# Kernel optimization log

Hardware: AMD Instinct MI355X
Metric: run time of the kernel (lower is better)

The kernel has to match this reference:

```python
import jax, jax.numpy as jnp
import numpy as np

B, M, N = 64, 100, 100
LAMBDA_COORD = 1.0
LAMBDA_CONF = 1.0
EPS = 1e-12


def _hungarian(cost):
    """O(n^3) Hungarian algorithm (potentials / e-maxx variant) on a square
    numpy cost matrix. Returns row_to_col assignment (length n)."""
    n = cost.shape[0]
    u = np.zeros(n + 1)
    v = np.zeros(n + 1)
    p = np.zeros(n + 1, dtype=np.int64)   # p[j] = row matched to column j
    way = np.zeros(n + 1, dtype=np.int64)
    for i in range(1, n + 1):
        p[0] = i
        j0 = 0
        minv = np.full(n + 1, np.inf)
        used = np.zeros(n + 1, dtype=bool)
        while True:
            used[j0] = True
            i0 = p[j0]
            js = np.nonzero(~used)[0]
            js = js[js > 0]
            cur = cost[i0 - 1, js - 1] - u[i0] - v[js]
            upd = cur < minv[js]
            minv[js] = np.where(upd, cur, minv[js])
            way[js] = np.where(upd, j0, way[js])
            j1 = js[np.argmin(minv[js])]
            delta = minv[j1]
            uj = np.nonzero(used)[0]
            u[p[uj]] += delta
            v[uj] -= delta
            minv[js] -= delta
            j0 = j1
            if p[j0] == 0:
                break
        while j0:
            j1 = way[j0]
            p[j0] = p[j1]
            j0 = j1
    row_to_col = np.full(n, -1, dtype=np.int64)
    for j in range(1, n + 1):
        row_to_col[p[j] - 1] = j - 1
    return row_to_col


def _match(pred_xy, target_xy, target_conf):
    """Host-side matching (mirrors the original's CPU round trip).
    Returns padded rows [B,P], cols [B,P] (cols index into the ORIGINAL target
    axis) and cnt [B] = number of matched pairs (min(M, K_valid))."""
    Bb, Mm, _ = pred_xy.shape
    Nn = target_xy.shape[1]
    P = min(Mm, Nn)
    rows = np.zeros((Bb, P), np.int64)
    cols = np.zeros((Bb, P), np.int64)
    cnt = np.zeros(Bb, np.int64)
    for b in range(Bb):
        valid = np.nonzero(target_conf[b] > 0.5)[0]
        K = valid.size
        if K == 0:
            continue
        tgt = target_xy[b, valid]                       # [K,2]
        cost = np.linalg.norm(pred_xy[b][:, None, :] - tgt[None, :, :], axis=-1)  # [M,K]
        n = max(Mm, K)
        sq = np.zeros((n, n))                           # zero-pad to square
        sq[:Mm, :K] = cost
        r2c = _hungarian(sq)
        k = 0
        for r in range(Mm):
            c = r2c[r]
            if 0 <= c < K:
                rows[b, k] = r
                cols[b, k] = valid[c]
                k += 1
        cnt[b] = k
    return rows, cols, cnt


def _loss(pred, target, rows, cols, cnt):
    Bb, P = rows.shape
    bidx = jnp.arange(Bb)[:, None]
    mp = pred[bidx, rows]                                # [B,P,3] matched preds
    mt = target[bidx, cols]                              # [B,P,3] matched tgts
    mask = (jnp.arange(P)[None, :] < cnt[:, None]).astype(pred.dtype)
    denom = jnp.maximum(cnt, 1).astype(pred.dtype)
    # per-batch F.mse_loss: mean over cnt*2 coord elements
    se = (((mp[..., :2] - mt[..., :2]) ** 2).sum(-1) * mask).sum(-1)
    loss_coord = jnp.where(cnt > 0, se / (2.0 * denom), 0.0).sum()
    # per-batch F.binary_cross_entropy: mean over cnt elements
    pconf = jnp.clip(mp[..., 2], EPS, 1.0 - EPS)
    tconf = mt[..., 2]
    bce = -(tconf * jnp.log(pconf) + (1.0 - tconf) * jnp.log1p(-pconf))
    loss_conf = jnp.where(cnt > 0, (bce * mask).sum(-1) / denom, 0.0).sum()
    return (LAMBDA_COORD * loss_coord + LAMBDA_CONF * loss_conf) / Bb


def setup_inputs() -> dict:
    key = jax.random.key(0)
    k1, k2 = jax.random.split(key)
    pred = jax.random.uniform(k1, (B, M, 3), dtype=jnp.float32)
    target = jax.random.uniform(k2, (B, N, 3), dtype=jnp.float32)
    return {"pred": pred, "target": target}


def reference(pred, target):
    pred_np = np.asarray(pred)
    tgt_np = np.asarray(target)
    rows, cols, cnt = _match(pred_np[..., :2], tgt_np[..., :2], tgt_np[..., 2])
    rows = jnp.asarray(rows)
    cols = jnp.asarray(cols)
    cnt = jnp.asarray(cnt)
    return _loss(pred, target, rows, cols, cnt)
```

## Files before the change

kernel.cpp:

```cpp
#include <hip/hip_runtime.h>
#include <math.h>

#define BATCH 64
#define MM 100
#define NN 100
#define ST 101
#define BIGCLAIM 0x7fffffff


__device__ __forceinline__ int readlane_i(int v, int lane) {
    return __builtin_amdgcn_readlane(v, lane);
}
__device__ __forceinline__ float readlane_f(float v, int lane) {
    return __int_as_float(__builtin_amdgcn_readlane(__float_as_int(v), lane));
}

template<int CTRL>
__device__ __forceinline__ float dpp_min_f32(float x) {
    int p = __builtin_amdgcn_update_dpp(__float_as_int(x), __float_as_int(x),
                                        CTRL, 0xF, 0xF, false);
    return fminf(x, __int_as_float(p));
}
__device__ __forceinline__ float wave_min_f32(float x) {
    x = dpp_min_f32<0xB1>(x);
    x = dpp_min_f32<0x4E>(x);
    x = dpp_min_f32<0x141>(x);
    x = dpp_min_f32<0x140>(x);
    x = dpp_min_f32<0x142>(x);
    x = dpp_min_f32<0x143>(x);
    return readlane_f(x, 63);
}


__global__ __launch_bounds__(128) void hungarian_loss_kernel(
        const float* __restrict__ pred, const float* __restrict__ target,
        double* __restrict__ ws) {
    const int b    = blockIdx.x;
    const int tid  = threadIdx.x;
    const int lane = tid & 63;
    const int wave = tid >> 6;
    const float* P = pred + b * MM * 3;
    const float* T = target + b * NN * 3;

    __shared__ float px[MM], py[MM], pc[MM];
    __shared__ float tvx[NN], tvy[NN], tvc[NN];
    __shared__ float Tc[NN * ST];
    __shared__ int   rmini[NN];
    __shared__ int   claimArr[MM + 1];
    __shared__ int   Ksh;

    float pxA = P[3*lane], pyA = P[3*lane+1];
    float pxB = 0.f, pyB = 0.f;
    const bool colBvalid = (lane + 64 < MM);
    if (colBvalid) { pxB = P[3*(lane+64)]; pyB = P[3*(lane+64)+1]; }

    if (wave == 0) {
        px[lane] = pxA; py[lane] = pyA; pc[lane] = P[3*lane+2];
        if (colBvalid) { px[lane+64]=pxB; py[lane+64]=pyB; pc[lane+64]=P[3*(lane+64)+2]; }
        float cxA=0.f, cyA=0.f, ccA=0.f, cxB=0.f, cyB=0.f, ccB=0.f;
        bool vA_=false, vB_=false;
        { cxA=T[3*lane]; cyA=T[3*lane+1]; ccA=T[3*lane+2]; vA_ = ccA > 0.5f; }
        if (lane + 64 < NN) {
            cxB=T[3*(lane+64)]; cyB=T[3*(lane+64)+1]; ccB=T[3*(lane+64)+2];
            vB_ = ccB > 0.5f;
        }
        unsigned long long mAv = __ballot(vA_);
        unsigned long long mBv = __ballot(vB_);
        int nA_ = __popcll(mAv);
        int K0  = nA_ + __popcll(mBv);
        unsigned long long below = (1ull << lane) - 1ull;
        if (vA_) { int q = __popcll(mAv & below);       tvx[q]=cxA; tvy[q]=cyA; tvc[q]=ccA; }
        if (vB_) { int q = nA_ + __popcll(mBv & below); tvx[q]=cxB; tvy[q]=cyB; tvc[q]=ccB; }
        if (lane == 0) Ksh = K0;
        claimArr[lane] = BIGCLAIM;
        if (lane + 64 <= MM) claimArr[lane + 64] = BIGCLAIM;
    }
    __syncthreads();
    const int K = Ksh;
    if (K == 0) { if (tid == 0) ws[b] = 0.0; return; }

    float txA = (lane < K)      ? tvx[lane]      : 0.f;
    float tyA = (lane < K)      ? tvy[lane]      : 0.f;
    float txB = (lane + 64 < K) ? tvx[lane + 64] : 0.f;
    float tyB = (lane + 64 < K) ? tvy[lane + 64] : 0.f;

    for (int c = wave; c < K; c += 2) {
        float tx = (c < 64) ? readlane_f(txA, c) : readlane_f(txB, c - 64);
        float ty = (c < 64) ? readlane_f(tyA, c) : readlane_f(tyB, c - 64);
        float dxA = __fsub_rn(pxA, tx), dyA = __fsub_rn(pyA, ty);
        float cA = __fsqrt_rn(__fadd_rn(__fmul_rn(dxA,dxA), __fmul_rn(dyA,dyA)));
        Tc[c*ST + lane] = cA;
        float cB = 1e30f;
        if (colBvalid) {
            float dxB = __fsub_rn(pxB, tx), dyB = __fsub_rn(pyB, ty);
            cB = __fsqrt_rn(__fadd_rn(__fmul_rn(dxB,dxB), __fmul_rn(dyB,dyB)));
            Tc[c*ST + lane + 64] = cB;
        }
        float m = wave_min_f32(fminf(cA, cB));
        unsigned long long eA = __ballot(cA == m);
        unsigned long long eB = __ballot(cB == m);
        int argc = eA ? ((int)__ffsll(eA) - 1) : ((int)__ffsll(eB) - 1 + 64);
        if (lane == 0) rmini[c] = argc;
    }
    __syncthreads();
    if (wave == 1) return;

    const float INF32 = __builtin_inff();
    const int jA = lane;
    const int jB = lane + 64;
    const bool validB = (jB <= MM);
    const int idxA = (jA >= 1) ? (jA - 1) : 0;
    const int idxB = validB ? (jB - 1) : (MM - 1);

    int rA = lane + 1, rB = lane + 65;
    int argA = 0, argB = 0;
    if (lane < K)      { argA = rmini[lane] + 1;      atomicMin(&claimArr[argA], rA); }
    if (lane + 64 < K) { argB = rmini[lane + 64] + 1; atomicMin(&claimArr[argB], rB); }
    __threadfence_block();
    int pA = 0, pB = 0;
    if (jA >= 1) { int c0 = claimArr[jA]; pA = (c0 != BIGCLAIM) ? c0 : 0; }
    if (validB)  { int c0 = claimArr[jB]; pB = (c0 != BIGCLAIM) ? c0 : 0; }
    bool freeA = (lane < K)      && (claimArr[argA] != rA);
    bool freeB = (lane + 64 < K) && (claimArr[argB] != rB);
    unsigned long long fA = __ballot(freeA);
    unsigned long long fB = __ballot(freeB);

    float vvA = 0.f, vvB = 0.f;

    unsigned long long dijA = 0ull, dijB = 0ull;
    for (int sweep = 0; sweep < 2; ++sweep) {
        unsigned long long curA = fA, curB = fB;
        fA = 0ull; fB = 0ull;
        while (curA | curB) {
            int r;
            if (curA) { r = (int)__ffsll(curA);      curA &= curA - 1; }
            else      { r = (int)__ffsll(curB) + 64; curB &= curB - 1; }

            float cA = Tc[(r-1)*ST + idxA];
            float cB = Tc[(r-1)*ST + idxB];
            float rcA = (jA >= 1) ? (cA - vvA) : INF32;
            float rcB = validB ? (cB - vvB) : INF32;
            float m1 = wave_min_f32(fminf(rcA, rcB));
            unsigned long long eA = __ballot(rcA == m1);
            unsigned long long eB = __ballot(rcB == m1);
            int j1 = eA ? ((int)__ffsll(eA) - 1) : ((int)__ffsll(eB) - 1 + 64);

            float rcA2 = (jA == j1) ? INF32 : rcA;
            float rcB2 = (jB == j1) ? INF32 : rcB;
            float m2 = wave_min_f32(fminf(rcA2, rcB2));

            int holder = (j1 < 64) ? readlane_i(pA, j1) : readlane_i(pB, j1 & 63);

            if (m1 < m2) {
                float dv = m2 - m1;
                if (jA == j1) { vvA -= dv; pA = r; }
                if (validB && jB == j1) { vvB -= dv; pB = r; }
                if (holder != 0) {
                    if (sweep == 0) {
                        if (holder <= 64) fA |= 1ull << (holder - 1);
                        else              fB |= 1ull << (holder - 65);
                    } else {
                        if (holder <= 64) dijA |= 1ull << (holder - 1);
                        else              dijB |= 1ull << (holder - 65);
                    }
                }
            } else {
                if (holder == 0) {
                    if (jA == j1) pA = r;
                    if (validB && jB == j1) pB = r;
                } else {
                    unsigned long long e2A = __ballot(rcA2 == m2);
                    unsigned long long e2B = __ballot(rcB2 == m2);
                    int j2 = e2A ? ((int)__ffsll(e2A) - 1)
                                 : ((int)__ffsll(e2B) - 1 + 64);
                    int h2 = (j2 < 64) ? readlane_i(pA, j2)
                                       : readlane_i(pB, j2 & 63);
                    if (h2 == 0) {
                        if (jA == j2) pA = r;
                        if (validB && jB == j2) pB = r;
                    } else {
                        if (sweep == 0) {
                            if (r <= 64) fA |= 1ull << (r - 1);
                            else         fB |= 1ull << (r - 65);
                        } else {
                            if (r <= 64) dijA |= 1ull << (r - 1);
                            else         dijB |= 1ull << (r - 65);
                        }
                    }
                }
            }
        }
    }

    while (dijA | dijB) {
        int r;
        if (dijA) { r = (int)__ffsll(dijA);      dijA &= dijA - 1; }
        else      { r = (int)__ffsll(dijB) + 64; dijB &= dijB - 1; }

        float minvA = INF32, minvB = INF32;
        int wayA = 0, wayB = 0;
        bool usedA = (lane == 0), usedB = false;
        float dpopA = 0.f, dpopB = 0.f;
        if (lane == 0) pA = r;
        int j0 = 0, jfree = -1;
        float dstar = 0.f;

        float cA_f = Tc[(r-1)*ST + idxA];
        float cB_f = Tc[(r-1)*ST + idxB];
        float S = 0.f;

        for (int it = 0; it <= MM; ++it) {
            float candA = INF32, candB = INF32;
            if (jA >= 1 && !usedA) {
                float t = (cA_f - vvA) + S;
                if (t < minvA) { minvA = t; wayA = j0; }
                candA = minvA;
            }
            if (validB && !usedB) {
                float t = (cB_f - vvB) + S;
                if (t < minvB) { minvB = t; wayB = j0; }
                candB = minvB;
            }

            float delta = wave_min_f32(fminf(candA, candB));
            unsigned long long eA = __ballot(candA == delta);
            unsigned long long eB = __ballot(candB == delta);
            int j1 = eA ? ((int)__ffsll(eA) - 1) : ((int)__ffsll(eB) - 1 + 64);

            if (jA == j1) { usedA = true; dpopA = delta; }
            if (jB == j1) { usedB = true; dpopB = delta; }

            int pa = readlane_i(pA, j1 & 63);
            int pb = readlane_i(pB, j1 & 63);
            int pj1 = (j1 < 64) ? pa : pb;
            if (pj1 == 0) { jfree = j1; dstar = delta; break; }

            float nxA = Tc[(pj1-1)*ST + idxA];
            float nxB = Tc[(pj1-1)*ST + idxB];
            float cjm = (j1 < 64) ? readlane_f(nxA, j1) : readlane_f(nxB, j1 & 63);
            float vjm = (j1 < 64) ? readlane_f(vvA, j1) : readlane_f(vvB, j1 & 63);
            S = (delta - cjm) + vjm;
            cA_f = nxA; cB_f = nxB;
            j0 = j1;
        }

        if (usedA && jA >= 1) vvA += dpopA - dstar;
        if (usedB)            vvB += dpopB - dstar;

        int jc = jfree;
        for (int s = 0; s <= MM && jc > 0; ++s) {
            int wa = readlane_i(wayA, jc & 63);
            int wb = readlane_i(wayB, jc & 63);
            int w  = (jc < 64) ? wa : wb;
            int pa = readlane_i(pA, w & 63);
            int pb = readlane_i(pB, w & 63);
            int pw = (w < 64) ? pa : pb;
            if (jA == jc) pA = pw;
            if (jB == jc) pB = pw;
            jc = w;
        }
    }

    double se = 0.0, bce = 0.0;
    if (jA >= 1 && pA > 0) {
        int rr = jA - 1, c = pA - 1;
        float dx = __fsub_rn(px[rr], tvx[c]);
        float dy = __fsub_rn(py[rr], tvy[c]);
        se = (double)dx*(double)dx + (double)dy*(double)dy;
        double pcv = (double)pc[rr];
        pcv = fmin(fmax(pcv, 1e-12), 1.0 - 1e-12);
        double tc = (double)tvc[c];
        bce = -(tc * log(pcv) + (1.0 - tc) * log1p(-pcv));
    }
    if (validB && pB > 0) {
        int rr = jB - 1, c = pB - 1;
        float dx = __fsub_rn(px[rr], tvx[c]);
        float dy = __fsub_rn(py[rr], tvy[c]);
        se += (double)dx*(double)dx + (double)dy*(double)dy;
        double pcv = (double)pc[rr];
        pcv = fmin(fmax(pcv, 1e-12), 1.0 - 1e-12);
        double tc = (double)tvc[c];
        bce += -(tc * log(pcv) + (1.0 - tc) * log1p(-pcv));
    }
    for (int m = 1; m < 64; m <<= 1) {
        se  += __shfl_xor(se,  m, 64);
        bce += __shfl_xor(bce, m, 64);
    }
    if (lane == 0) ws[b] = se / (2.0 * (double)K) + bce / (double)K;
}

__global__ __launch_bounds__(64) void final_reduce(const double* __restrict__ ws,
                                                   float* __restrict__ out) {
    double v = ws[threadIdx.x];
    for (int m = 1; m < 64; m <<= 1) v += __shfl_xor(v, m, 64);
    if (threadIdx.x == 0) out[0] = (float)(v / (double)BATCH);
}

extern "C" void kernel_launch(void* const* d_in, const int* in_sizes, int n_in,
                              void* d_out, int out_size, void* d_ws, size_t ws_size,
                              hipStream_t stream) {
    const float* pred   = (const float*)d_in[0];
    const float* target = (const float*)d_in[1];
    double* ws = (double*)d_ws;
    float* out = (float*)d_out;
    hungarian_loss_kernel<<<dim3(BATCH), dim3(128), 0, stream>>>(pred, target, ws);
    final_reduce<<<dim3(1), dim3(64), 0, stream>>>(ws, out);
}
```

Measured before the change: 53.63 us.

## Split Hungarian kernel into two stages and use packed-key wave argmin

Replaces the float wave-min plus ballot argmin with a single unsigned min over packed keys (order-preserving float bits with the low 7 bits replaced by the column index). The auction sweep now always takes the second-best value instead of branching on ties. The kernel is split into a stage that builds costs and runs the auction and a stage that rebuilds the cost matrix and runs Dijkstra augmentation, passing state through workspace memory. This cuts the number of reductions per step but adds a launch, recomputes the cost matrix, and truncates key precision, which can change tie-breaking and the final matching.

```diff
diff --git a/kernel.cpp b/kernel.cpp
--- a/kernel.cpp
+++ b/kernel.cpp
@@ -6,6 +6,8 @@
 #define NN 100
 #define ST 101
 #define BIGCLAIM 0x7fffffff
+#define WS_STATE_OFF 512
+#define WS_STRIDE   1024
 
 
 __device__ __forceinline__ int readlane_i(int v, int lane) {
@@ -15,26 +17,31 @@
     return __int_as_float(__builtin_amdgcn_readlane(__float_as_int(v), lane));
 }
 
+__device__ __forceinline__ unsigned pack_key(float x, int col) {
+    unsigned u = __float_as_uint(x);
+    u ^= ((unsigned)((int)u >> 31)) | 0x80000000u;
+    return (u & 0xFFFFFF80u) | (unsigned)col;
+}
+
 template<int CTRL>
-__device__ __forceinline__ float dpp_min_f32(float x) {
-    int p = __builtin_amdgcn_update_dpp(__float_as_int(x), __float_as_int(x),
-                                        CTRL, 0xF, 0xF, false);
-    return fminf(x, __int_as_float(p));
-}
-__device__ __forceinline__ float wave_min_f32(float x) {
-    x = dpp_min_f32<0xB1>(x);
-    x = dpp_min_f32<0x4E>(x);
-    x = dpp_min_f32<0x141>(x);
-    x = dpp_min_f32<0x140>(x);
-    x = dpp_min_f32<0x142>(x);
-    x = dpp_min_f32<0x143>(x);
-    return readlane_f(x, 63);
-}
-
-
-__global__ __launch_bounds__(128) void hungarian_loss_kernel(
+__device__ __forceinline__ unsigned dpp_min_u32(unsigned x) {
+    int p = __builtin_amdgcn_update_dpp((int)x, (int)x, CTRL, 0xF, 0xF, false);
+    unsigned up = (unsigned)p;
+    return (x < up) ? x : up;
+}
+__device__ __forceinline__ unsigned wave_min_u32(unsigned x) {
+    x = dpp_min_u32<0xB1>(x);
+    x = dpp_min_u32<0x4E>(x);
+    x = dpp_min_u32<0x141>(x);
+    x = dpp_min_u32<0x140>(x);
+    x = dpp_min_u32<0x142>(x);
+    x = dpp_min_u32<0x143>(x);
+    return (unsigned)readlane_i((int)x, 63);
+}
+
+__global__ __launch_bounds__(128) void hung_stage1(
         const float* __restrict__ pred, const float* __restrict__ target,
-        double* __restrict__ ws) {
+        char* __restrict__ wsbase) {
     const int b    = blockIdx.x;
     const int tid  = threadIdx.x;
     const int lane = tid & 63;
@@ -42,8 +49,7 @@
     const float* P = pred + b * MM * 3;
     const float* T = target + b * NN * 3;
 
-    __shared__ float px[MM], py[MM], pc[MM];
-    __shared__ float tvx[NN], tvy[NN], tvc[NN];
+    __shared__ float tvx[NN], tvy[NN];
     __shared__ float Tc[NN * ST];
     __shared__ int   rmini[NN];
     __shared__ int   claimArr[MM + 1];
@@ -54,30 +60,30 @@
     const bool colBvalid = (lane + 64 < MM);
     if (colBvalid) { pxB = P[3*(lane+64)]; pyB = P[3*(lane+64)+1]; }
 
+    int* st = (int*)(wsbase + WS_STATE_OFF + (size_t)b * WS_STRIDE);
+
     if (wave == 0) {
-        px[lane] = pxA; py[lane] = pyA; pc[lane] = P[3*lane+2];
-        if (colBvalid) { px[lane+64]=pxB; py[lane+64]=pyB; pc[lane+64]=P[3*(lane+64)+2]; }
-        float cxA=0.f, cyA=0.f, ccA=0.f, cxB=0.f, cyB=0.f, ccB=0.f;
-        bool vA_=false, vB_=false;
-        { cxA=T[3*lane]; cyA=T[3*lane+1]; ccA=T[3*lane+2]; vA_ = ccA > 0.5f; }
+        float cxA=T[3*lane], cyA=T[3*lane+1], ccA=T[3*lane+2];
+        bool vA_ = ccA > 0.5f;
+        float cxB=0.f, cyB=0.f; bool vB_=false;
         if (lane + 64 < NN) {
-            cxB=T[3*(lane+64)]; cyB=T[3*(lane+64)+1]; ccB=T[3*(lane+64)+2];
-            vB_ = ccB > 0.5f;
+            cxB=T[3*(lane+64)]; cyB=T[3*(lane+64)+1];
+            vB_ = T[3*(lane+64)+2] > 0.5f;
         }
         unsigned long long mAv = __ballot(vA_);
         unsigned long long mBv = __ballot(vB_);
         int nA_ = __popcll(mAv);
         int K0  = nA_ + __popcll(mBv);
         unsigned long long below = (1ull << lane) - 1ull;
-        if (vA_) { int q = __popcll(mAv & below);       tvx[q]=cxA; tvy[q]=cyA; tvc[q]=ccA; }
-        if (vB_) { int q = nA_ + __popcll(mBv & below); tvx[q]=cxB; tvy[q]=cyB; tvc[q]=ccB; }
+        if (vA_) { int q = __popcll(mAv & below);       tvx[q]=cxA; tvy[q]=cyA; }
+        if (vB_) { int q = nA_ + __popcll(mBv & below); tvx[q]=cxB; tvy[q]=cyB; }
         if (lane == 0) Ksh = K0;
         claimArr[lane] = BIGCLAIM;
         if (lane + 64 <= MM) claimArr[lane + 64] = BIGCLAIM;
     }
     __syncthreads();
     const int K = Ksh;
-    if (K == 0) { if (tid == 0) ws[b] = 0.0; return; }
+    if (K == 0) { if (tid == 0) st[0] = 0; return; }
 
     float txA = (lane < K)      ? tvx[lane]      : 0.f;
     float tyA = (lane < K)      ? tvy[lane]      : 0.f;
@@ -90,17 +96,16 @@
         float dxA = __fsub_rn(pxA, tx), dyA = __fsub_rn(pyA, ty);
         float cA = __fsqrt_rn(__fadd_rn(__fmul_rn(dxA,dxA), __fmul_rn(dyA,dyA)));
         Tc[c*ST + lane] = cA;
-        float cB = 1e30f;
+        unsigned kB = 0xFFFFFFFFu;
         if (colBvalid) {
             float dxB = __fsub_rn(pxB, tx), dyB = __fsub_rn(pyB, ty);
-            cB = __fsqrt_rn(__fadd_rn(__fmul_rn(dxB,dxB), __fmul_rn(dyB,dyB)));
+            float cB = __fsqrt_rn(__fadd_rn(__fmul_rn(dxB,dxB), __fmul_rn(dyB,dyB)));
             Tc[c*ST + lane + 64] = cB;
-        }
-        float m = wave_min_f32(fminf(cA, cB));
-        unsigned long long eA = __ballot(cA == m);
-        unsigned long long eB = __ballot(cB == m);
-        int argc = eA ? ((int)__ffsll(eA) - 1) : ((int)__ffsll(eB) - 1 + 64);
-        if (lane == 0) rmini[c] = argc;
+            kB = pack_key(cB, lane + 64);
+        }
+        unsigned kA = pack_key(cA, lane);
+        unsigned k = wave_min_u32(kA < kB ? kA : kB);
+        if (lane == 0) rmini[c] = (int)(k & 127u);
     }
     __syncthreads();
     if (wave == 1) return;
@@ -140,57 +145,125 @@
             float cB = Tc[(r-1)*ST + idxB];
             float rcA = (jA >= 1) ? (cA - vvA) : INF32;
             float rcB = validB ? (cB - vvB) : INF32;
-            float m1 = wave_min_f32(fminf(rcA, rcB));
-            unsigned long long eA = __ballot(rcA == m1);
-            unsigned long long eB = __ballot(rcB == m1);
-            int j1 = eA ? ((int)__ffsll(eA) - 1) : ((int)__ffsll(eB) - 1 + 64);
-
-            float rcA2 = (jA == j1) ? INF32 : rcA;
-            float rcB2 = (jB == j1) ? INF32 : rcB;
-            float m2 = wave_min_f32(fminf(rcA2, rcB2));
+            unsigned kA = pack_key(rcA, jA);
+            unsigned kB = pack_key(rcB, jB);
+            unsigned k1 = wave_min_u32(kA < kB ? kA : kB);
+            int j1 = (int)(k1 & 127u);
+            unsigned kA2 = (jA == j1) ? 0xFFFFFFFFu : kA;
+            unsigned kB2 = (jB == j1) ? 0xFFFFFFFFu : kB;
+            unsigned k2 = wave_min_u32(kA2 < kB2 ? kA2 : kB2);
+            int j2 = (int)(k2 & 127u);
+
+            float v1a = readlane_f(rcA, j1 & 63), v1b = readlane_f(rcB, j1 & 63);
+            float val1 = (j1 < 64) ? v1a : v1b;
+            float v2a = readlane_f(rcA, j2 & 63), v2b = readlane_f(rcB, j2 & 63);
+            float val2 = (j2 < 64) ? v2a : v2b;
+            float dv = fmaxf(val2 - val1, 0.f);
 
             int holder = (j1 < 64) ? readlane_i(pA, j1) : readlane_i(pB, j1 & 63);
-
-            if (m1 < m2) {
-                float dv = m2 - m1;
-                if (jA == j1) { vvA -= dv; pA = r; }
-                if (validB && jB == j1) { vvB -= dv; pB = r; }
-                if (holder != 0) {
-                    if (sweep == 0) {
-                        if (holder <= 64) fA |= 1ull << (holder - 1);
-                        else              fB |= 1ull << (holder - 65);
-                    } else {
-                        if (holder <= 64) dijA |= 1ull << (holder - 1);
-                        else              dijB |= 1ull << (holder - 65);
-                    }
-                }
-            } else {
-                if (holder == 0) {
-                    if (jA == j1) pA = r;
-                    if (validB && jB == j1) pB = r;
+            if (jA == j1) { vvA -= dv; pA = r; }
+            if (validB && jB == j1) { vvB -= dv; pB = r; }
+            if (holder != 0) {
+                if (sweep == 0) {
+                    if (holder <= 64) fA |= 1ull << (holder - 1);
+                    else              fB |= 1ull << (holder - 65);
                 } else {
-                    unsigned long long e2A = __ballot(rcA2 == m2);
-                    unsigned long long e2B = __ballot(rcB2 == m2);
-                    int j2 = e2A ? ((int)__ffsll(e2A) - 1)
-                                 : ((int)__ffsll(e2B) - 1 + 64);
-                    int h2 = (j2 < 64) ? readlane_i(pA, j2)
-                                       : readlane_i(pB, j2 & 63);
-                    if (h2 == 0) {
-                        if (jA == j2) pA = r;
-                        if (validB && jB == j2) pB = r;
-                    } else {
-                        if (sweep == 0) {
-                            if (r <= 64) fA |= 1ull << (r - 1);
-                            else         fB |= 1ull << (r - 65);
-                        } else {
-                            if (r <= 64) dijA |= 1ull << (r - 1);
-                            else         dijB |= 1ull << (r - 65);
-                        }
-                    }
+                    if (holder <= 64) dijA |= 1ull << (holder - 1);
+                    else              dijB |= 1ull << (holder - 65);
                 }
             }
         }
     }
+
+    if (lane == 0) {
+        st[0] = K;
+        *(unsigned long long*)(st + 2) = dijA;
+        *(unsigned long long*)(st + 4) = dijB;
+    }
+    int*   pArr  = st + 6;
+    float* vvArr = (float*)(st + 6 + 101);
+    pArr[lane] = pA;  vvArr[lane] = vvA;
+    if (validB) { pArr[jB] = pB; vvArr[jB] = vvB; }
+}
+
+__global__ __launch_bounds__(128) void hung_stage2(
+        const float* __restrict__ pred, const float* __restrict__ target,
+        char* __restrict__ wsbase, double* __restrict__ wsloss) {
+    const int b    = blockIdx.x;
+    const int tid  = threadIdx.x;
+    const int lane = tid & 63;
+    const int wave = tid >> 6;
+    const float* P = pred + b * MM * 3;
+    const float* T = target + b * NN * 3;
+
+    __shared__ float px[MM], py[MM], pc[MM];
+    __shared__ float tvx[NN], tvy[NN], tvc[NN];
+    __shared__ float Tc[NN * ST];
+    __shared__ int   Ksh;
+
+    float pxA = P[3*lane], pyA = P[3*lane+1];
+    float pxB = 0.f, pyB = 0.f;
+    const bool colBvalid = (lane + 64 < MM);
+    if (colBvalid) { pxB = P[3*(lane+64)]; pyB = P[3*(lane+64)+1]; }
+
+    const int* st = (const int*)(wsbase + WS_STATE_OFF + (size_t)b * WS_STRIDE);
+
+    if (wave == 0) {
+        px[lane] = pxA; py[lane] = pyA; pc[lane] = P[3*lane+2];
+        if (colBvalid) { px[lane+64]=pxB; py[lane+64]=pyB; pc[lane+64]=P[3*(lane+64)+2]; }
+        float cxA=T[3*lane], cyA=T[3*lane+1], ccA=T[3*lane+2];
+        bool vA_ = ccA > 0.5f;
+        float cxB=0.f, cyB=0.f, ccB=0.f; bool vB_=false;
+        if (lane + 64 < NN) {
+            cxB=T[3*(lane+64)]; cyB=T[3*(lane+64)+1]; ccB=T[3*(lane+64)+2];
+            vB_ = ccB > 0.5f;
+        }
+        unsigned long long mAv = __ballot(vA_);
+        unsigned long long mBv = __ballot(vB_);
+        int nA_ = __popcll(mAv);
+        int K0  = nA_ + __popcll(mBv);
+        unsigned long long below = (1ull << lane) - 1ull;
+        if (vA_) { int q = __popcll(mAv & below);       tvx[q]=cxA; tvy[q]=cyA; tvc[q]=ccA; }
+        if (vB_) { int q = nA_ + __popcll(mBv & below); tvx[q]=cxB; tvy[q]=cyB; tvc[q]=ccB; }
+        if (lane == 0) Ksh = K0;
+    }
+    __syncthreads();
+    const int K = Ksh;
+    if (K == 0) { if (tid == 0) wsloss[b] = 0.0; return; }
+
+    float txA = (lane < K)      ? tvx[lane]      : 0.f;
+    float tyA = (lane < K)      ? tvy[lane]      : 0.f;
+    float txB = (lane + 64 < K) ? tvx[lane + 64] : 0.f;
+    float tyB = (lane + 64 < K) ? tvy[lane + 64] : 0.f;
+
+    const int jA = lane;
+    const int jB = lane + 64;
+    const bool validB = (jB <= MM);
+    unsigned long long dijA = *(const unsigned long long*)(st + 2);
+    unsigned long long dijB = *(const unsigned long long*)(st + 4);
+    const int*   pArr  = st + 6;
+    const float* vvArr = (const float*)(st + 6 + 101);
+    int pA = pArr[lane];
+    int pB = validB ? pArr[jB] : 0;
+    float vvA = vvArr[lane];
+    float vvB = validB ? vvArr[jB] : 0.f;
+
+    for (int c = wave; c < K; c += 2) {
+        float tx = (c < 64) ? readlane_f(txA, c) : readlane_f(txB, c - 64);
+        float ty = (c < 64) ? readlane_f(tyA, c) : readlane_f(tyB, c - 64);
+        float dxA = __fsub_rn(pxA, tx), dyA = __fsub_rn(pyA, ty);
+        Tc[c*ST + lane] = __fsqrt_rn(__fadd_rn(__fmul_rn(dxA,dxA), __fmul_rn(dyA,dyA)));
+        if (colBvalid) {
+            float dxB = __fsub_rn(pxB, tx), dyB = __fsub_rn(pyB, ty);
+            Tc[c*ST + lane + 64] = __fsqrt_rn(__fadd_rn(__fmul_rn(dxB,dxB), __fmul_rn(dyB,dyB)));
+        }
+    }
+    __syncthreads();
+    if (wave == 1) return;
+
+    const float INF32 = __builtin_inff();
+    const int idxA = (jA >= 1) ? (jA - 1) : 0;
+    const int idxB = validB ? (jB - 1) : (MM - 1);
 
     while (dijA | dijB) {
         int r;
@@ -210,22 +283,20 @@
         float S = 0.f;
 
         for (int it = 0; it <= MM; ++it) {
-            float candA = INF32, candB = INF32;
             if (jA >= 1 && !usedA) {
                 float t = (cA_f - vvA) + S;
                 if (t < minvA) { minvA = t; wayA = j0; }
-                candA = minvA;
             }
             if (validB && !usedB) {
                 float t = (cB_f - vvB) + S;
                 if (t < minvB) { minvB = t; wayB = j0; }
-                candB = minvB;
             }
-
-            float delta = wave_min_f32(fminf(candA, candB));
-            unsigned long long eA = __ballot(candA == delta);
-            unsigned long long eB = __ballot(candB == delta);
-            int j1 = eA ? ((int)__ffsll(eA) - 1) : ((int)__ffsll(eB) - 1 + 64);
+            unsigned kA = (jA >= 1 && !usedA) ? pack_key(minvA, jA) : 0xFFFFFFFFu;
+            unsigned kB = (validB && !usedB) ? pack_key(minvB, jB) : 0xFFFFFFFFu;
+            unsigned k1 = wave_min_u32(kA < kB ? kA : kB);
+            int j1 = (int)(k1 & 127u);
+            float da = readlane_f(minvA, j1 & 63), db = readlane_f(minvB, j1 & 63);
+            float delta = (j1 < 64) ? da : db;
 
             if (jA == j1) { usedA = true; dpopA = delta; }
             if (jB == j1) { usedB = true; dpopB = delta; }
@@ -286,7 +357,7 @@
         se  += __shfl_xor(se,  m, 64);
         bce += __shfl_xor(bce, m, 64);
     }
-    if (lane == 0) ws[b] = se / (2.0 * (double)K) + bce / (double)K;
+    if (lane == 0) wsloss[b] = se / (2.0 * (double)K) + bce / (double)K;
 }
 
 __global__ __launch_bounds__(64) void final_reduce(const double* __restrict__ ws,
@@ -301,8 +372,10 @@
                               hipStream_t stream) {
     const float* pred   = (const float*)d_in[0];
     const float* target = (const float*)d_in[1];
-    double* ws = (double*)d_ws;
-    float* out = (float*)d_out;
-    hungarian_loss_kernel<<<dim3(BATCH), dim3(128), 0, stream>>>(pred, target, ws);
-    final_reduce<<<dim3(1), dim3(64), 0, stream>>>(ws, out);
-}
+    char*   wsb = (char*)d_ws;
+    double* wsl = (double*)d_ws;
+    float*  out = (float*)d_out;
+    hung_stage1<<<dim3(BATCH), dim3(128), 0, stream>>>(pred, target, wsb);
+    hung_stage2<<<dim3(BATCH), dim3(128), 0, stream>>>(pred, target, wsb, wsl);
+    final_reduce<<<dim3(1), dim3(64), 0, stream>>>(wsl, out);
+}
```

Measured after the change: 58.96 us. +9.9%, slower.
